# Performance work log

Hardware: AMD Instinct MI355X
Metric: run time of the kernel (lower is better)

The kernel has to match this reference:

```python
import jax, jax.numpy as jnp
import numpy as np

VOCAB = 100000
EMB = 128
B = 16384
C = 20
N = 20


def setup_inputs() -> dict:
    key = jax.random.key(0)
    k1, k2, k3, k4, k5 = jax.random.split(key, 5)
    initrange = 1.0 / EMB
    return {
        "pos_target": jax.random.randint(k1, (B,), 0, VOCAB),
        "pos_contexts": jax.random.randint(k2, (B, C), 0, VOCAB),
        "pos_negatives": jax.random.randint(k3, (B, N), 0, VOCAB),
        "context_table": jax.random.uniform(k4, (VOCAB, EMB), jnp.float32, -initrange, initrange),
        "output_table": jax.random.uniform(k5, (VOCAB, EMB), jnp.float32, -initrange, initrange),
    }


def reference(pos_target, pos_contexts, pos_negatives, context_table, output_table):
    # gather + sum over context window: [B, C, D] -> [B, D]
    mean_contexts = jnp.sum(context_table[pos_contexts], axis=1)
    emb_target = output_table[pos_target]           # [B, D]
    emb_negs = output_table[pos_negatives]          # [B, N, D]

    # positive objective: dot(mean_contexts, emb_target) per row
    pos_score = jnp.clip(jnp.sum(mean_contexts * emb_target, axis=1), -10.0, 10.0)
    objective = -jax.nn.log_sigmoid(pos_score)      # [B]

    # negative objective: bmm [B,N,D] x [B,D] -> [B,N]
    neg_score = jnp.clip(jnp.einsum("bnd,bd->bn", emb_negs, mean_contexts), -10.0, 10.0)
    neg_objective = -jnp.sum(jax.nn.log_sigmoid(-neg_score), axis=1)  # [B]

    return jnp.mean(objective + neg_objective)
```

## Files before the change

kernel.cpp:

```cpp
#include <hip/hip_runtime.h>
#include <math.h>

#define VOCAB 100000
#define EMB   128
#define BATCH 16384
#define CTX   20
#define NEG   20
#define NSCORE (NEG + 1)

__device__ __forceinline__ float dot4(float4 a, float4 b) {
    return fmaf(a.x, b.x, fmaf(a.y, b.y, fmaf(a.z, b.z, a.w * b.w)));
}

__device__ __forceinline__ float fast_softplus(float x) {
    return __logf(1.0f + __expf(x));
}

__global__ __launch_bounds__(256, 8) void cbow_loss_kernel(
    const int*   __restrict__ pos_target,
    const int*   __restrict__ pos_contexts,
    const int*   __restrict__ pos_negatives,
    const float* __restrict__ context_table,
    const float* __restrict__ output_table,
    float*       __restrict__ out)
{
    const int tid  = threadIdx.x;
    const int lane = tid & 63;
    const int wave = tid >> 6;
    const int half = lane >> 5;
    const int sub  = lane & 31;

    const int row = blockIdx.x * 8 + wave * 2 + half;

    const float4* ctab = (const float4*)context_table;
    const float4* otab = (const float4*)output_table;

    int cidx = (sub < CTX) ? pos_contexts[row * CTX + sub] : 0;
    int sidx = (sub == 0) ? pos_target[row]
             : (sub <= NEG ? pos_negatives[row * NEG + sub - 1] : 0);

    auto ctx_idx = [&](int j) { return __shfl(cidx, j, 32); };
    auto sc_idx  = [&](int j) { return __shfl(sidx, j, 32); };

    float4 acc = make_float4(0.f, 0.f, 0.f, 0.f);
    {
        float4 buf[2][5];
#pragma unroll
        for (int j = 0; j < 5; ++j)
            buf[0][j] = ctab[ctx_idx(j) * 32 + sub];
#pragma unroll
        for (int g = 0; g < 4; ++g) {
            if (g + 1 < 4) {
#pragma unroll
                for (int j = 0; j < 5; ++j)
                    buf[(g + 1) & 1][j] = ctab[ctx_idx((g + 1) * 5 + j) * 32 + sub];
            }
#pragma unroll
            for (int j = 0; j < 5; ++j) {
                const float4 a = buf[g & 1][j];
                acc.x += a.x; acc.y += a.y; acc.z += a.z; acc.w += a.w;
            }
        }
    }

    float part[NSCORE];
    {
        float4 sbuf[2][7];
#pragma unroll
        for (int j = 0; j < 7; ++j)
            sbuf[0][j] = otab[sc_idx(j) * 32 + sub];
#pragma unroll
        for (int g = 0; g < 3; ++g) {
            if (g + 1 < 3) {
#pragma unroll
                for (int j = 0; j < 7; ++j)
                    sbuf[(g + 1) & 1][j] = otab[sc_idx((g + 1) * 7 + j) * 32 + sub];
            }
#pragma unroll
            for (int j = 0; j < 7; ++j)
                part[g * 7 + j] = dot4(acc, sbuf[g & 1][j]);
        }
    }

#pragma unroll
    for (int s = 16; s >= 1; s >>= 1) {
#pragma unroll
        for (int n = 0; n < NSCORE; ++n) part[n] += __shfl_xor(part[n], s);
    }

    __shared__ float sdata[8];
    if (sub == 0) {
        float ps = fminf(fmaxf(part[0], -10.f), 10.f);
        float loss = fast_softplus(-ps);
#pragma unroll
        for (int n = 1; n < NSCORE; ++n) {
            float ns = fminf(fmaxf(part[n], -10.f), 10.f);
            loss += fast_softplus(ns);
        }
        sdata[wave * 2 + half] = loss;
    }
    __syncthreads();

    if (tid == 0) {
        float s = 0.f;
#pragma unroll
        for (int i = 0; i < 8; ++i) s += sdata[i];
        atomicAdd(out, s * (1.0f / (float)BATCH));
    }
}

extern "C" void kernel_launch(void* const* d_in, const int* in_sizes, int n_in,
                              void* d_out, int out_size, void* d_ws, size_t ws_size,
                              hipStream_t stream) {
    const int*   pos_target    = (const int*)d_in[0];
    const int*   pos_contexts  = (const int*)d_in[1];
    const int*   pos_negatives = (const int*)d_in[2];
    const float* context_table = (const float*)d_in[3];
    const float* output_table  = (const float*)d_in[4];
    float* out = (float*)d_out;

    hipMemsetAsync(out, 0, sizeof(float), stream);

    const int rows_per_block = 8;
    const int grid = BATCH / rows_per_block;
    cbow_loss_kernel<<<grid, 256, 0, stream>>>(
        pos_target, pos_contexts, pos_negatives, context_table, output_table, out);
}
```

Before: 168.9 us.

## Map one row per wavefront with float2 loads and all gathers issued upfront

Each 64-lane wave now handles one batch row instead of two half-waves each taking a row, so every lane loads float2 instead of float4. All 20 context and 21 score gathers are issued before any arithmetic, replacing the double-buffered grouped loads, to raise memory-level parallelism. The reduction grows to six shuffle steps, and the block count doubles with four rows per block. The trade-off is narrower per-lane loads, twice as many waves, and higher register pressure from holding 41 float2 values.

```diff
diff --git a/kernel.cpp b/kernel.cpp
--- a/kernel.cpp
+++ b/kernel.cpp
@@ -8,15 +8,11 @@
 #define NEG   20
 #define NSCORE (NEG + 1)
 
-__device__ __forceinline__ float dot4(float4 a, float4 b) {
-    return fmaf(a.x, b.x, fmaf(a.y, b.y, fmaf(a.z, b.z, a.w * b.w)));
-}
-
 __device__ __forceinline__ float fast_softplus(float x) {
     return __logf(1.0f + __expf(x));
 }
 
-__global__ __launch_bounds__(256, 8) void cbow_loss_kernel(
+__global__ __launch_bounds__(256, 4) void cbow_loss_kernel(
     const int*   __restrict__ pos_target,
     const int*   __restrict__ pos_contexts,
     const int*   __restrict__ pos_negatives,
@@ -27,69 +23,48 @@
     const int tid  = threadIdx.x;
     const int lane = tid & 63;
     const int wave = tid >> 6;
-    const int half = lane >> 5;
-    const int sub  = lane & 31;
+    const int row  = blockIdx.x * 4 + wave;
 
-    const int row = blockIdx.x * 8 + wave * 2 + half;
+    const float2* ctab = (const float2*)context_table;
+    const float2* otab = (const float2*)output_table;
 
-    const float4* ctab = (const float4*)context_table;
-    const float4* otab = (const float4*)output_table;
+    int ci = (lane < CTX) ? pos_contexts[row * CTX + lane] : 0;
+    int si = (lane == 0) ? pos_target[row]
+           : (lane <= NEG ? pos_negatives[row * NEG + lane - 1] : 0);
 
-    int cidx = (sub < CTX) ? pos_contexts[row * CTX + sub] : 0;
-    int sidx = (sub == 0) ? pos_target[row]
-             : (sub <= NEG ? pos_negatives[row * NEG + sub - 1] : 0);
+    float2 cbuf[CTX];
+#pragma unroll
+    for (int j = 0; j < CTX; ++j) {
+        const int idx = __shfl(ci, j);
+        cbuf[j] = ctab[idx * 64 + lane];
+    }
+    float2 sbuf[NSCORE];
+#pragma unroll
+    for (int j = 0; j < NSCORE; ++j) {
+        const int idx = __shfl(si, j);
+        sbuf[j] = otab[idx * 64 + lane];
+    }
 
-    auto ctx_idx = [&](int j) { return __shfl(cidx, j, 32); };
-    auto sc_idx  = [&](int j) { return __shfl(sidx, j, 32); };
-
-    float4 acc = make_float4(0.f, 0.f, 0.f, 0.f);
-    {
-        float4 buf[2][5];
+    float2 acc = make_float2(0.f, 0.f);
 #pragma unroll
-        for (int j = 0; j < 5; ++j)
-            buf[0][j] = ctab[ctx_idx(j) * 32 + sub];
-#pragma unroll
-        for (int g = 0; g < 4; ++g) {
-            if (g + 1 < 4) {
-#pragma unroll
-                for (int j = 0; j < 5; ++j)
-                    buf[(g + 1) & 1][j] = ctab[ctx_idx((g + 1) * 5 + j) * 32 + sub];
-            }
-#pragma unroll
-            for (int j = 0; j < 5; ++j) {
-                const float4 a = buf[g & 1][j];
-                acc.x += a.x; acc.y += a.y; acc.z += a.z; acc.w += a.w;
-            }
-        }
+    for (int j = 0; j < CTX; ++j) {
+        acc.x += cbuf[j].x;
+        acc.y += cbuf[j].y;
     }
 
     float part[NSCORE];
-    {
-        float4 sbuf[2][7];
 #pragma unroll
-        for (int j = 0; j < 7; ++j)
-            sbuf[0][j] = otab[sc_idx(j) * 32 + sub];
+    for (int j = 0; j < NSCORE; ++j)
+        part[j] = fmaf(acc.x, sbuf[j].x, acc.y * sbuf[j].y);
+
 #pragma unroll
-        for (int g = 0; g < 3; ++g) {
-            if (g + 1 < 3) {
+    for (int s = 32; s >= 1; s >>= 1) {
 #pragma unroll
-                for (int j = 0; j < 7; ++j)
-                    sbuf[(g + 1) & 1][j] = otab[sc_idx((g + 1) * 7 + j) * 32 + sub];
-            }
-#pragma unroll
-            for (int j = 0; j < 7; ++j)
-                part[g * 7 + j] = dot4(acc, sbuf[g & 1][j]);
-        }
+        for (int j = 0; j < NSCORE; ++j) part[j] += __shfl_xor(part[j], s);
     }
 
-#pragma unroll
-    for (int s = 16; s >= 1; s >>= 1) {
-#pragma unroll
-        for (int n = 0; n < NSCORE; ++n) part[n] += __shfl_xor(part[n], s);
-    }
-
-    __shared__ float sdata[8];
-    if (sub == 0) {
+    __shared__ float sdata[4];
+    if (lane == 0) {
         float ps = fminf(fmaxf(part[0], -10.f), 10.f);
         float loss = fast_softplus(-ps);
 #pragma unroll
@@ -97,14 +72,12 @@
             float ns = fminf(fmaxf(part[n], -10.f), 10.f);
             loss += fast_softplus(ns);
         }
-        sdata[wave * 2 + half] = loss;
+        sdata[wave] = loss;
     }
     __syncthreads();
 
     if (tid == 0) {
-        float s = 0.f;
-#pragma unroll
-        for (int i = 0; i < 8; ++i) s += sdata[i];
+        float s = sdata[0] + sdata[1] + sdata[2] + sdata[3];
         atomicAdd(out, s * (1.0f / (float)BATCH));
     }
 }
@@ -121,7 +94,7 @@
 
     hipMemsetAsync(out, 0, sizeof(float), stream);
 
-    const int rows_per_block = 8;
+    const int rows_per_block = 4;
     const int grid = BATCH / rows_per_block;
     cbow_loss_kernel<<<grid, 256, 0, stream>>>(
         pos_target, pos_contexts, pos_negatives, context_table, output_table, out);
```

Result: slower. 173.1 us (+2.5%).
